# Performance work log

Measured on AMD Instinct MI355X. Metric: run time of the kernel, lower is better.

## Reference

```python
import jax, jax.numpy as jnp
import numpy as np

# Fixed multi-scale pyramid (H, W) per level -- static config, closed over.
SPATIAL_SHAPES = [(100, 100), (50, 50), (25, 25), (13, 13)]
D_MODEL, N_HEADS, N_LEVELS, N_POINTS = 256, 8, 4, 4
C_HEAD = D_MODEL // N_HEADS
B = 2
NUM_KEYS = sum(h * w for h, w in SPATIAL_SHAPES)  # 13294
NUM_QUERIES = NUM_KEYS


def setup_inputs() -> dict:
    key = jax.random.key(0)
    ks = jax.random.split(key, 12)
    d = D_MODEL
    return {
        "query": jax.random.normal(ks[0], (B, NUM_QUERIES, d), jnp.float32),
        "reference_points": jax.random.uniform(ks[1], (B, NUM_QUERIES, N_LEVELS, 2), jnp.float32),
        "input_flatten": jax.random.normal(ks[2], (B, NUM_KEYS, d), jnp.float32),
        "Wv": jax.random.normal(ks[3], (d, d), jnp.float32) * 0.02,
        "bv": jnp.zeros((d,), jnp.float32),
        "Ws": jax.random.normal(ks[4], (d, N_HEADS * N_LEVELS * N_POINTS * 2), jnp.float32) * 0.01,
        "bs": jax.random.normal(ks[5], (N_HEADS * N_LEVELS * N_POINTS * 2,), jnp.float32),
        "Wa": jax.random.normal(ks[6], (d, N_HEADS * N_LEVELS * N_POINTS), jnp.float32) * 0.02,
        "ba": jnp.zeros((N_HEADS * N_LEVELS * N_POINTS,), jnp.float32),
        "Wo": jax.random.normal(ks[7], (d, d), jnp.float32) * 0.02,
        "bo": jnp.zeros((d,), jnp.float32),
    }


def _bilinear_sample(v, grid, H, W):
    """torch.F.grid_sample(mode='bilinear', padding_mode='zeros', align_corners=False).
    v: (N, H, W, C); grid: (N, M, 2) with (x, y) in [-1, 1]. Returns (N, M, C)."""
    x = (grid[..., 0] + 1.0) * (W * 0.5) - 0.5
    y = (grid[..., 1] + 1.0) * (H * 0.5) - 0.5
    x0 = jnp.floor(x)
    y0 = jnp.floor(y)
    dx = x - x0
    dy = y - y0
    x0i = x0.astype(jnp.int32)
    y0i = y0.astype(jnp.int32)
    vflat = v.reshape(v.shape[0], H * W, v.shape[-1])

    def gather(xi, yi):
        valid = (xi >= 0) & (xi < W) & (yi >= 0) & (yi < H)
        idx = jnp.clip(yi, 0, H - 1) * W + jnp.clip(xi, 0, W - 1)  # (N, M)
        g = jnp.take_along_axis(vflat, idx[..., None], axis=1)
        return g * valid[..., None]

    v00 = gather(x0i, y0i)
    v10 = gather(x0i + 1, y0i)
    v01 = gather(x0i, y0i + 1)
    v11 = gather(x0i + 1, y0i + 1)
    return (v00 * ((1 - dx) * (1 - dy))[..., None]
            + v10 * (dx * (1 - dy))[..., None]
            + v01 * ((1 - dx) * dy)[..., None]
            + v11 * (dx * dy)[..., None])


def _ms_deform_attn(value, sampling_locations, attention_weights):
    # value: (B, NK, H, Ch); loc: (B, NQ, H, L, P, 2); w: (B, NQ, H, L, P)
    grids = 2.0 * sampling_locations - 1.0
    splits = np.cumsum([h * w for h, w in SPATIAL_SHAPES])[:-1]
    value_list = jnp.split(value, splits, axis=1)
    acc = 0.0
    for lvl, (H, W) in enumerate(SPATIAL_SHAPES):
        # (B, H*W, heads, Ch) -> (B*heads, H, W, Ch)
        v_l = value_list[lvl].reshape(B, H, W, N_HEADS, C_HEAD)
        v_l = v_l.transpose(0, 3, 1, 2, 4).reshape(B * N_HEADS, H, W, C_HEAD)
        # (B, NQ, heads, P, 2) -> (B*heads, NQ*P, 2)
        g_l = grids[:, :, :, lvl].transpose(0, 2, 1, 3, 4).reshape(B * N_HEADS, -1, 2)
        samp = _bilinear_sample(v_l, g_l, H, W)  # (B*heads, NQ*P, Ch)
        samp = samp.reshape(B, N_HEADS, -1, N_POINTS, C_HEAD)
        w_l = attention_weights[:, :, :, lvl].transpose(0, 2, 1, 3)  # (B, heads, NQ, P)
        acc = acc + jnp.einsum("bhqpc,bhqp->bhqc", samp, w_l)
    return acc.transpose(0, 2, 1, 3).reshape(B, -1, D_MODEL)  # (B, NQ, d_model)


def reference(query, reference_points, input_flatten, Wv, bv, Ws, bs, Wa, ba, Wo, bo):
    value = (input_flatten @ Wv + bv).reshape(B, NUM_KEYS, N_HEADS, C_HEAD)
    offsets = (query @ Ws + bs).reshape(B, NUM_QUERIES, N_HEADS, N_LEVELS, N_POINTS, 2)
    attw = jax.nn.softmax(
        (query @ Wa + ba).reshape(B, NUM_QUERIES, N_HEADS, N_LEVELS * N_POINTS), axis=-1
    ).reshape(B, NUM_QUERIES, N_HEADS, N_LEVELS, N_POINTS)
    # NOTE: module divides by [H, W] (not [W, H]) -- replicated faithfully.
    normalizer = jnp.asarray(SPATIAL_SHAPES, jnp.float32)  # (L, 2) = (H, W)
    normalizer = jnp.clip(normalizer, 1.0)
    loc = reference_points[:, :, None, :, None, :] + offsets / normalizer[None, None, None, :, None, :]
    out = _ms_deform_attn(value, loc, attw)
    return out @ Wo + bo
```

## Files before the change

### kernel.cpp

```cpp
#include <hip/hip_runtime.h>
#include <hip/hip_bf16.h>
#include <hip/hip_fp16.h>
#include <math.h>

#define B_  2
#define NQ  13294
#define NK  13294
#define M_  (B_ * NK)
#define MT  32
#define GX  ((M_ + MT - 1) / MT)

typedef __bf16 bf16x8 __attribute__((ext_vector_type(8)));
typedef float f32x4 __attribute__((ext_vector_type(4)));

static __device__ __forceinline__ f32x4 mfma16(bf16x8 a, bf16x8 b, f32x4 c) {
  return __builtin_amdgcn_mfma_f32_16x16x32_bf16(a, b, c, 0, 0, 0);
}

static __device__ __forceinline__ void pack_one(
    const float* __restrict__ W1, const float* __restrict__ W2,
    int N1, int Ntot, __hip_bfloat16* __restrict__ out, int g) {
  int lane = g & 63;
  int n_sub = (g >> 6) & 3;
  int kt = (g >> 8) & 7;
  int bn = g >> 11;
  int n = bn * 64 + n_sub * 16 + (lane & 15);
  int k0 = kt * 32 + (lane >> 4) * 8;
  const float* src; int nn, Ns;
  if (n < N1) { src = W1; nn = n; Ns = N1; }
  else        { src = W2; nn = n - N1; Ns = Ntot - N1; }
  bf16x8 v;
#pragma unroll
  for (int j = 0; j < 8; ++j) v[j] = (__bf16)src[(size_t)(k0 + j) * Ns + nn];
  *(bf16x8*)(out + (size_t)g * 8) = v;
}

__global__ __launch_bounds__(256) void pack_all(
    const float* __restrict__ Wv, const float* __restrict__ Ws,
    const float* __restrict__ Wa, const float* __restrict__ Wo,
    __hip_bfloat16* __restrict__ wv_p, __hip_bfloat16* __restrict__ wsa_p,
    __hip_bfloat16* __restrict__ wo_p) {
  const int b = blockIdx.x, t = threadIdx.x;
  if (b < 32)       pack_one(Wv, Wv, 256, 256, wv_p,  b * 256 + t);
  else if (b < 80)  pack_one(Ws, Wa, 256, 384, wsa_p, (b - 32) * 256 + t);
  else              pack_one(Wo, Wo, 256, 256, wo_p,  (b - 80) * 256 + t);
}

static __device__ __forceinline__ int bin_of(const float* refp, int b, int q) {
  const size_t base = (((size_t)b * NQ + q) * 4) * 2;
  float rx = refp[base + 0], ry = refp[base + 1];
  int bx = (int)(rx * 32.f); bx = bx < 0 ? 0 : (bx > 31 ? 31 : bx);
  int by = (int)(ry * 32.f); by = by < 0 ? 0 : (by > 31 ? 31 : by);
  return b * 1024 + by * 32 + bx;
}

__global__ __launch_bounds__(256) void hist_k(
    const float* __restrict__ refp, unsigned int* __restrict__ hist) {
  int i = blockIdx.x * 256 + threadIdx.x;
  if (i >= 2 * NQ) return;
  int b = i >= NQ; int q = i - b * NQ;
  atomicAdd(&hist[bin_of(refp, b, q)], 1u);
}

__global__ __launch_bounds__(256) void scan_k(
    const unsigned int* __restrict__ hist, unsigned int* __restrict__ cursor) {
  __shared__ unsigned int lds[256];
  const int t = threadIdx.x;
  unsigned int v[8], s = 0;
#pragma unroll
  for (int j = 0; j < 8; ++j) { v[j] = hist[t * 8 + j]; s += v[j]; }
  lds[t] = s; __syncthreads();
  for (int off = 1; off < 256; off <<= 1) {
    unsigned int x = (t >= off) ? lds[t - off] : 0u;
    __syncthreads();
    lds[t] += x;
    __syncthreads();
  }
  unsigned int base = lds[t] - s;
#pragma unroll
  for (int j = 0; j < 8; ++j) { cursor[t * 8 + j] = base; base += v[j]; }
}

__global__ __launch_bounds__(256) void scatter_k(
    const float* __restrict__ refp, unsigned int* __restrict__ cursor,
    unsigned int* __restrict__ perm) {
  int i = blockIdx.x * 256 + threadIdx.x;
  if (i >= 2 * NQ) return;
  int b = i >= NQ; int q = i - b * NQ;
  unsigned int pos = atomicAdd(&cursor[bin_of(refp, b, q)], 1u);
  perm[pos] = (unsigned int)q;
}

#define CSTR 68

__global__ __launch_bounds__(128) void gemm_mt(
    const float* __restrict__ inpf, const float* __restrict__ query,
    const bf16x8* __restrict__ wv_p, const bf16x8* __restrict__ wsa_p,
    const float* __restrict__ bv, const float* __restrict__ bs,
    const float* __restrict__ ba,
    __hip_bfloat16* __restrict__ value, __half* __restrict__ params) {
  __shared__ bf16x8 As[8 * 2 * 64];
  __shared__ float  Cs[2 * 16 * CSTR];

  const int t = threadIdx.x;
  const int bm = blockIdx.x * MT;
  const int lane = t & 63, wid = t >> 6;
  const int mode = blockIdx.y;

  {
    const int r = t >> 2;
    const int row = bm + r;
    const int sm = r >> 4;
    const int lb = r & 15;
    const bool ok = row < M_;
    const float* Af = (mode == 0) ? inpf : query;
    const float* ap = Af + (size_t)row * 256 + (t & 3) * 64;
#pragma unroll
    for (int gi = 0; gi < 8; ++gi) {
      float4 u = make_float4(0.f,0.f,0.f,0.f), v = make_float4(0.f,0.f,0.f,0.f);
      if (ok) { u = *(const float4*)(ap + gi * 8); v = *(const float4*)(ap + gi * 8 + 4); }
      bf16x8 w;
      w[0]=(__bf16)u.x; w[1]=(__bf16)u.y; w[2]=(__bf16)u.z; w[3]=(__bf16)u.w;
      w[4]=(__bf16)v.x; w[5]=(__bf16)v.y; w[6]=(__bf16)v.z; w[7]=(__bf16)v.w;
      int k8 = (t & 3) * 8 + gi;
      As[((k8 >> 2) * 2 + sm) * 64 + lb + ((k8 & 3) << 4)] = w;
    }
  }
  __syncthreads();

  const bf16x8* Bp = (mode == 0) ? wv_p : wsa_p;
  const int NB = (mode == 1) ? 6 : 4;
  float* Cw = &Cs[wid * 16 * CSTR];

  for (int nb = wid; nb < NB; nb += 2) {
    const int colbase = nb * 64;
    const bf16x8* bpn = Bp + (size_t)nb * 2048;

    f32x4 acc[2][4] = {};
#pragma unroll
    for (int kt = 0; kt < 8; ++kt) {
      bf16x8 a0 = As[(kt * 2 + 0) * 64 + lane];
      bf16x8 a1 = As[(kt * 2 + 1) * 64 + lane];
#pragma unroll
      for (int n = 0; n < 4; ++n) {
        bf16x8 b = bpn[(kt * 4 + n) * 64 + lane];
        acc[0][n] = mfma16(a0, b, acc[0][n]);
        acc[1][n] = mfma16(a1, b, acc[1][n]);
      }
    }

#pragma unroll
    for (int m = 0; m < 2; ++m) {
#pragma unroll
      for (int n = 0; n < 4; ++n)
#pragma unroll
        for (int rg = 0; rg < 4; ++rg)
          Cw[((lane >> 4) * 4 + rg) * CSTR + n * 16 + (lane & 15)] = acc[m][n][rg];

      const int r = lane >> 2;
      const int c0 = (lane & 3) * 16;
      const int row = bm + m * 16 + r;
      const int col = colbase + c0;
      float vv[16];
      *(float4*)&vv[0]  = *(float4*)&Cw[r * CSTR + c0 + 0];
      *(float4*)&vv[4]  = *(float4*)&Cw[r * CSTR + c0 + 4];
      *(float4*)&vv[8]  = *(float4*)&Cw[r * CSTR + c0 + 8];
      *(float4*)&vv[12] = *(float4*)&Cw[r * CSTR + c0 + 12];

      if (mode == 0) {
        const float* bias = bv + col;
        bf16x8 o0, o1;
#pragma unroll
        for (int j = 0; j < 8; ++j) {
          o0[j] = (__bf16)(vv[j] + bias[j]);
          o1[j] = (__bf16)(vv[8 + j] + bias[8 + j]);
        }
        if (row < M_) {
          *(bf16x8*)(value + (size_t)row * 256 + col + 0) = o0;
          *(bf16x8*)(value + (size_t)row * 256 + col + 8) = o1;
        }
      } else {
        const float* bias = (col < 256) ? (bs + col) : (ba + col - 256);
        uint4 st0, st1;
        __half2 h;
        h = __floats2half2_rn(vv[0] + bias[0],  vv[1] + bias[1]);  st0.x = *(unsigned*)&h;
        h = __floats2half2_rn(vv[2] + bias[2],  vv[3] + bias[3]);  st0.y = *(unsigned*)&h;
        h = __floats2half2_rn(vv[4] + bias[4],  vv[5] + bias[5]);  st0.z = *(unsigned*)&h;
        h = __floats2half2_rn(vv[6] + bias[6],  vv[7] + bias[7]);  st0.w = *(unsigned*)&h;
        h = __floats2half2_rn(vv[8] + bias[8],  vv[9] + bias[9]);  st1.x = *(unsigned*)&h;
        h = __floats2half2_rn(vv[10] + bias[10], vv[11] + bias[11]); st1.y = *(unsigned*)&h;
        h = __floats2half2_rn(vv[12] + bias[12], vv[13] + bias[13]); st1.z = *(unsigned*)&h;
        h = __floats2half2_rn(vv[14] + bias[14], vv[15] + bias[15]); st1.w = *(unsigned*)&h;
        if (row < M_) {
          *(uint4*)(params + (size_t)row * 384 + col + 0) = st0;
          *(uint4*)(params + (size_t)row * 384 + col + 8) = st1;
        }
      }
    }
  }
}

#define CS 66

__global__ __launch_bounds__(512, 3) void sampler(
    const float* __restrict__ refp, const __half* __restrict__ params,
    const __hip_bfloat16* __restrict__ value, const bf16x8* __restrict__ wo_p,
    const float* __restrict__ bo, const unsigned int* __restrict__ perm,
    float* __restrict__ outp) {
  __shared__ unsigned int combo[128 * CS];
  __shared__ unsigned int qmap[16];

  const int c  = blockIdx.x & 7;
  const int kk = blockIdx.x >> 3;
  const int bb = c >> 2;
  const int qb = (c & 3) * 208 + kk;
  const int q0 = qb * 16;

  const int t = threadIdx.x;
  if (t < 16)
    qmap[t] = (q0 + t < NQ) ? perm[(size_t)bb * NQ + q0 + t] : 0xFFFFFFFFu;
  __syncthreads();

  {
    const int cqi = t >> 5;
    const int chh = (t >> 2) & 7;
    const int cl  = t & 3;
    const float DIMF[4]  = {100.f, 50.f, 25.f, 13.f};
    const int   LSTART[4] = {0, 10000, 12500, 13125};
    const float dimf  = DIMF[cl];
    const int   Wd    = (int)dimf;
    const int   lbase = LSTART[cl];

    const unsigned int qreal = qmap[cqi];
    const bool valid = qreal != 0xFFFFFFFFu;
    const size_t row = (size_t)bb * NQ + (valid ? qreal : 0);
    const __half* pr = params + row * 384;

    union { uint4 u[2]; __half h[16]; } LG;
    LG.u[0] = *(const uint4*)(pr + 256 + chh * 16);
    LG.u[1] = *(const uint4*)(pr + 256 + chh * 16 + 8);
    float lgf[16];
#pragma unroll
    for (int j = 0; j < 16; ++j) lgf[j] = __half2float(LG.h[j]);
    float m = lgf[0];
#pragma unroll
    for (int j = 1; j < 16; ++j) m = fmaxf(m, lgf[j]);
    float s = 0.f;
#pragma unroll
    for (int j = 0; j < 16; ++j) s += __expf(lgf[j] - m);
    const float inv = valid ? 1.f / s : 0.f;

    const float rx = refp[(row * 4 + cl) * 2 + 0];
    const float ry = refp[(row * 4 + cl) * 2 + 1];
    union { uint4 u; __half h[8]; } OF;
    OF.u = *(const uint4*)(pr + chh * 32 + cl * 8);
    unsigned int* cb = &combo[(cqi * 8 + chh) * CS + cl * 16];

#pragma unroll
    for (int p = 0; p < 4; ++p) {
      const float wa = __expf(lgf[cl * 4 + p] - m) * inv;
      const float x = rx * dimf + __half2float(OF.h[p * 2 + 0]) - 0.5f;
      const float y = ry * dimf + __half2float(OF.h[p * 2 + 1]) - 0.5f;
      const float xf = floorf(x), yf = floorf(y);
      const float dx = x - xf, dy = y - yf;
      const int x0 = (int)xf, y0 = (int)yf;

      float wxl = 1.f - dx, wxh = dx;
      int xa;
      if (x0 >= 0 && x0 <= Wd - 2)      { xa = x0; }
      else if (x0 == -1)                { xa = 0;      wxl = dx;       wxh = 0.f; }
      else if (x0 == Wd - 1)            { xa = Wd - 2; wxl = 0.f;      wxh = 1.f - dx; }
      else                              { xa = 0;      wxl = 0.f;      wxh = 0.f; }

#pragma unroll
      for (int r = 0; r < 2; ++r) {
        const int yr = y0 + r;
        const float wy = r ? dy : (1.f - dy);
        const bool vy = (yr >= 0) && (yr < Wd);
        const float wl = vy ? wa * wy * wxl : 0.f;
        const float wh = vy ? wa * wy * wxh : 0.f;
        const int idx = lbase + (vy ? yr : 0) * Wd + xa;
        const unsigned int w2 = ((__float_as_uint(wl) + 0x8000u) & 0xffff0000u)
                              | ((__float_as_uint(wh) + 0x8000u) >> 16);
        cb[(p * 2 + r) * 2 + 0] = w2;
        cb[(p * 2 + r) * 2 + 1] = (unsigned)idx;
      }
    }
  }
  __syncthreads();

  const int lane = t & 63;
  const int wid  = t >> 6;

  {
    const int q2 = lane >> 5;
    const int gh = (lane >> 2) & 7;
    const int gs = lane & 3;
    const int qw = wid * 2 + q2;
    const int rr = qw * 8 + gh;
    const char* vb = (const char*)value;
    const unsigned int voff0 = (unsigned int)bb * (NK * 512u) + (unsigned)(gh * 64 + gs * 16);
    const uint2* cb = (const uint2*)&combo[rr * CS];

    float a0=0.f,a1=0.f,a2=0.f,a3=0.f,a4=0.f,a5=0.f,a6=0.f,a7=0.f;
#pragma unroll 2
    for (int e = 0; e < 32; ++e) {
      const uint2 u = cb[e];
      const float wl = __uint_as_float(u.x & 0xffff0000u);
      const float wh = __uint_as_float(u.x << 16);
      const char* pv = vb + (size_t)(voff0 + (u.y << 9));
      const uint4 v0 = *(const uint4*)(pv);
      const uint4 v1 = *(const uint4*)(pv + 512);
      a0 += wl * __uint_as_float(v0.x << 16);
      a1 += wl * __uint_as_float(v0.x & 0xffff0000u);
      a2 += wl * __uint_as_float(v0.y << 16);
      a3 += wl * __uint_as_float(v0.y & 0xffff0000u);
      a4 += wl * __uint_as_float(v0.z << 16);
      a5 += wl * __uint_as_float(v0.z & 0xffff0000u);
      a6 += wl * __uint_as_float(v0.w << 16);
      a7 += wl * __uint_as_float(v0.w & 0xffff0000u);
      a0 += wh * __uint_as_float(v1.x << 16);
      a1 += wh * __uint_as_float(v1.x & 0xffff0000u);
      a2 += wh * __uint_as_float(v1.y << 16);
      a3 += wh * __uint_as_float(v1.y & 0xffff0000u);
      a4 += wh * __uint_as_float(v1.z << 16);
      a5 += wh * __uint_as_float(v1.z & 0xffff0000u);
      a6 += wh * __uint_as_float(v1.w << 16);
      a7 += wh * __uint_as_float(v1.w & 0xffff0000u);
    }
    bf16x8 o;
    o[0]=(__bf16)a0; o[1]=(__bf16)a1; o[2]=(__bf16)a2; o[3]=(__bf16)a3;
    o[4]=(__bf16)a4; o[5]=(__bf16)a5; o[6]=(__bf16)a6; o[7]=(__bf16)a7;
    *(bf16x8*)(&combo[rr * CS + (rr & 1) * 2 + gs * 4]) = o;
  }
  __syncthreads();

  {
    const int ql = lane & 15;
    const int hi = lane >> 4;
    const unsigned int* abase = combo + ql * (8 * CS) + hi * 4;
    const int cbk = wid >> 1, sp = wid & 1;
    const bf16x8* bpn = wo_p + (size_t)cbk * 2048;
    f32x4 oacc[2] = {};
#pragma unroll
    for (int kt = 0; kt < 8; ++kt) {
      bf16x8 a = *(const bf16x8*)(abase + kt * CS + (kt & 1) * 2);
#pragma unroll
      for (int n = 0; n < 2; ++n)
        oacc[n] = mfma16(a, bpn[(kt * 4 + sp * 2 + n) * 64 + lane], oacc[n]);
    }
#pragma unroll
    for (int n = 0; n < 2; ++n) {
      const int col = cbk * 64 + sp * 32 + n * 16 + ql;
      const float bias = bo[col];
#pragma unroll
      for (int rg = 0; rg < 4; ++rg) {
        const int qi = hi * 4 + rg;
        const unsigned int qreal = qmap[qi];
        if (qreal != 0xFFFFFFFFu)
          outp[((size_t)bb * NQ + qreal) * 256 + col] = oacc[n][rg] + bias;
      }
    }
  }
}

extern "C" void kernel_launch(void* const* d_in, const int* in_sizes, int n_in,
                              void* d_out, int out_size, void* d_ws, size_t ws_size,
                              hipStream_t stream) {
  const float* query = (const float*)d_in[0];
  const float* refp  = (const float*)d_in[1];
  const float* inpf  = (const float*)d_in[2];
  const float* Wv    = (const float*)d_in[3];
  const float* bv    = (const float*)d_in[4];
  const float* Ws    = (const float*)d_in[5];
  const float* bs    = (const float*)d_in[6];
  const float* Wa    = (const float*)d_in[7];
  const float* ba    = (const float*)d_in[8];
  const float* Wo    = (const float*)d_in[9];
  const float* bo    = (const float*)d_in[10];
  float* out = (float*)d_out;

  char* w = (char*)d_ws;
  __hip_bfloat16* value  = (__hip_bfloat16*)w;            w += (size_t)(M_ + 1) * 256 * 2;
  __half*         params = (__half*)w;                    w += (size_t)M_ * 384 * 2;
  __hip_bfloat16* wv_p   = (__hip_bfloat16*)w;            w += 256 * 256 * 2;
  __hip_bfloat16* wsa_p  = (__hip_bfloat16*)w;            w += 256 * 384 * 2;
  __hip_bfloat16* wo_p   = (__hip_bfloat16*)w;            w += 256 * 256 * 2;
  unsigned int*   hist   = (unsigned int*)w;              w += 2048 * 4;
  unsigned int*   cursor = (unsigned int*)w;              w += 2048 * 4;
  unsigned int*   perm   = (unsigned int*)w;

  hipMemsetAsync(hist, 0, 2048 * 4, stream);

  const int sg = (2 * NQ + 255) / 256;
  hist_k<<<sg, 256, 0, stream>>>(refp, hist);
  scan_k<<<1, 256, 0, stream>>>(hist, cursor);
  scatter_k<<<sg, 256, 0, stream>>>(refp, cursor, perm);

  pack_all<<<112, 256, 0, stream>>>(Wv, Ws, Wa, Wo, wv_p, wsa_p, wo_p);

  gemm_mt<<<dim3(GX, 2), 128, 0, stream>>>(
      inpf, query, (const bf16x8*)wv_p, (const bf16x8*)wsa_p,
      bv, bs, ba, value, params);

  sampler<<<1664, 512, 0, stream>>>(refp, params, value,
                                    (const bf16x8*)wo_p, bo, perm, out);
}
```

Baseline: 116.3 us.

## Fuse weight packing, histogram, scan and scatter into one persistent kernel

Merges the pack, histogram, scan and scatter kernels into a single 104-block kernel. The blocks synchronise through a software grid barrier built on an atomic counter, which is zeroed by the existing memset. This removes three kernel launches and their inter-kernel gaps from a short prep phase. The barrier relies on all 104 blocks being co-resident, and the scan step now runs on one block while the other blocks spin.

Measured after the change: 129.6 us. 1.11x slower.

```diff
diff --git a/kernel.cpp b/kernel.cpp
--- a/kernel.cpp
+++ b/kernel.cpp
@@ -9,6 +9,7 @@
 #define M_  (B_ * NK)
 #define MT  32
 #define GX  ((M_ + MT - 1) / MT)
+#define PREPB 104
 
 typedef __bf16 bf16x8 __attribute__((ext_vector_type(8)));
 typedef float f32x4 __attribute__((ext_vector_type(4)));
@@ -35,17 +36,6 @@
   *(bf16x8*)(out + (size_t)g * 8) = v;
 }
 
-__global__ __launch_bounds__(256) void pack_all(
-    const float* __restrict__ Wv, const float* __restrict__ Ws,
-    const float* __restrict__ Wa, const float* __restrict__ Wo,
-    __hip_bfloat16* __restrict__ wv_p, __hip_bfloat16* __restrict__ wsa_p,
-    __hip_bfloat16* __restrict__ wo_p) {
-  const int b = blockIdx.x, t = threadIdx.x;
-  if (b < 32)       pack_one(Wv, Wv, 256, 256, wv_p,  b * 256 + t);
-  else if (b < 80)  pack_one(Ws, Wa, 256, 384, wsa_p, (b - 32) * 256 + t);
-  else              pack_one(Wo, Wo, 256, 256, wo_p,  (b - 80) * 256 + t);
-}
-
 static __device__ __forceinline__ int bin_of(const float* refp, int b, int q) {
   const size_t base = (((size_t)b * NQ + q) * 4) * 2;
   float rx = refp[base + 0], ry = refp[base + 1];
@@ -54,41 +44,67 @@
   return b * 1024 + by * 32 + bx;
 }
 
-__global__ __launch_bounds__(256) void hist_k(
-    const float* __restrict__ refp, unsigned int* __restrict__ hist) {
-  int i = blockIdx.x * 256 + threadIdx.x;
-  if (i >= 2 * NQ) return;
-  int b = i >= NQ; int q = i - b * NQ;
-  atomicAdd(&hist[bin_of(refp, b, q)], 1u);
-}
-
-__global__ __launch_bounds__(256) void scan_k(
-    const unsigned int* __restrict__ hist, unsigned int* __restrict__ cursor) {
-  __shared__ unsigned int lds[256];
+static __device__ __forceinline__ void gbar(unsigned* cnt, unsigned target) {
+  __syncthreads();
+  if (threadIdx.x == 0) {
+    __threadfence();
+    atomicAdd(cnt, 1u);
+    while (__hip_atomic_load(cnt, __ATOMIC_RELAXED, __HIP_MEMORY_SCOPE_AGENT) < target) {}
+    __threadfence();
+  }
+  __syncthreads();
+}
+
+__global__ __launch_bounds__(256) void prep_k(
+    const float* __restrict__ Wv, const float* __restrict__ Ws,
+    const float* __restrict__ Wa, const float* __restrict__ Wo,
+    const float* __restrict__ refp,
+    __hip_bfloat16* __restrict__ wv_p, __hip_bfloat16* __restrict__ wsa_p,
+    __hip_bfloat16* __restrict__ wo_p,
+    unsigned* __restrict__ hist, unsigned* __restrict__ cursor,
+    unsigned* __restrict__ perm, unsigned* __restrict__ cnt) {
+  __shared__ unsigned lds[256];
   const int t = threadIdx.x;
-  unsigned int v[8], s = 0;
-#pragma unroll
-  for (int j = 0; j < 8; ++j) { v[j] = hist[t * 8 + j]; s += v[j]; }
-  lds[t] = s; __syncthreads();
-  for (int off = 1; off < 256; off <<= 1) {
-    unsigned int x = (t >= off) ? lds[t - off] : 0u;
-    __syncthreads();
-    lds[t] += x;
-    __syncthreads();
-  }
-  unsigned int base = lds[t] - s;
-#pragma unroll
-  for (int j = 0; j < 8; ++j) { cursor[t * 8 + j] = base; base += v[j]; }
-}
-
-__global__ __launch_bounds__(256) void scatter_k(
-    const float* __restrict__ refp, unsigned int* __restrict__ cursor,
-    unsigned int* __restrict__ perm) {
-  int i = blockIdx.x * 256 + threadIdx.x;
-  if (i >= 2 * NQ) return;
-  int b = i >= NQ; int q = i - b * NQ;
-  unsigned int pos = atomicAdd(&cursor[bin_of(refp, b, q)], 1u);
-  perm[pos] = (unsigned int)q;
+  const int gid = blockIdx.x * 256 + t;
+  const int nthr = PREPB * 256;
+
+  for (int g = gid; g < 28672; g += nthr) {
+    if (g < 8192)       pack_one(Wv, Wv, 256, 256, wv_p, g);
+    else if (g < 20480) pack_one(Ws, Wa, 256, 384, wsa_p, g - 8192);
+    else                pack_one(Wo, Wo, 256, 256, wo_p, g - 20480);
+  }
+  for (int i = gid; i < 2 * NQ; i += nthr) {
+    int b = i >= NQ; int q = i - b * NQ;
+    atomicAdd(&hist[bin_of(refp, b, q)], 1u);
+  }
+  gbar(cnt, 1 * PREPB);
+
+  if (blockIdx.x == 0) {
+    unsigned v[8], s = 0;
+#pragma unroll
+    for (int j = 0; j < 8; ++j) {
+      v[j] = __hip_atomic_load(&hist[t * 8 + j], __ATOMIC_RELAXED,
+                               __HIP_MEMORY_SCOPE_AGENT);
+      s += v[j];
+    }
+    lds[t] = s; __syncthreads();
+    for (int off = 1; off < 256; off <<= 1) {
+      unsigned x = (t >= off) ? lds[t - off] : 0u;
+      __syncthreads();
+      lds[t] += x;
+      __syncthreads();
+    }
+    unsigned base = lds[t] - s;
+#pragma unroll
+    for (int j = 0; j < 8; ++j) { cursor[t * 8 + j] = base; base += v[j]; }
+  }
+  gbar(cnt, 2 * PREPB);
+
+  for (int i = gid; i < 2 * NQ; i += nthr) {
+    int b = i >= NQ; int q = i - b * NQ;
+    unsigned pos = atomicAdd(&cursor[bin_of(refp, b, q)], 1u);
+    perm[pos] = (unsigned)q;
+  }
 }
 
 #define CSTR 68
@@ -387,17 +403,15 @@
   __hip_bfloat16* wsa_p  = (__hip_bfloat16*)w;            w += 256 * 384 * 2;
   __hip_bfloat16* wo_p   = (__hip_bfloat16*)w;            w += 256 * 256 * 2;
   unsigned int*   hist   = (unsigned int*)w;              w += 2048 * 4;
+  unsigned int*   cnt    = (unsigned int*)w;              w += 16 * 4;
   unsigned int*   cursor = (unsigned int*)w;              w += 2048 * 4;
   unsigned int*   perm   = (unsigned int*)w;
 
-  hipMemsetAsync(hist, 0, 2048 * 4, stream);
-
-  const int sg = (2 * NQ + 255) / 256;
-  hist_k<<<sg, 256, 0, stream>>>(refp, hist);
-  scan_k<<<1, 256, 0, stream>>>(hist, cursor);
-  scatter_k<<<sg, 256, 0, stream>>>(refp, cursor, perm);
-
-  pack_all<<<112, 256, 0, stream>>>(Wv, Ws, Wa, Wo, wv_p, wsa_p, wo_p);
+  hipMemsetAsync(hist, 0, (2048 + 16) * 4, stream);
+
+  prep_k<<<PREPB, 256, 0, stream>>>(Wv, Ws, Wa, Wo, refp,
+                                    wv_p, wsa_p, wo_p,
+                                    hist, cursor, perm, cnt);
 
   gemm_mt<<<dim3(GX, 2), 128, 0, stream>>>(
       inpf, query, (const bf16x8*)wv_p, (const bf16x8*)wsa_p,
```
